# Kernel tuning notes

Measured on AMD Instinct MI355X. Metric: run time of the kernel, lower is better.

Reference implementation:

```python
import jax, jax.numpy as jnp
import numpy as np

B, N, CIN, COUT, K, P = 32, 3072, 32, 8, 3, 4
N2 = N // P


def _lap(key, n):
    a = jax.random.normal(key, (n, n), dtype=jnp.float32)
    # symmetric, spectral radius ~1 (Chebyshev-rescaled Laplacian stand-in)
    return 0.35 * (a + a.T) / jnp.sqrt(jnp.float32(n))


def setup_inputs() -> dict:
    key = jax.random.key(0)
    ks = iter(jax.random.split(key, 40))
    d = {}
    d['x'] = jax.random.normal(next(ks), (B, N, CIN), dtype=jnp.float32)
    d['L0'] = _lap(next(ks), N)
    d['L1'] = _lap(next(ks), N2)

    def cheb_p(k, cin, cout):
        w = jax.random.normal(k, (K, cin, cout), dtype=jnp.float32) * (1.0 / np.sqrt(K * cin))
        return w, jnp.zeros((cout,), jnp.float32)

    def bn_p(c):
        return jnp.ones((c,), jnp.float32), jnp.zeros((c,), jnp.float32)

    d['w11'], d['b11'] = cheb_p(next(ks), CIN, 64); d['g11'], d['be11'] = bn_p(64)
    d['w13'], d['b13'] = cheb_p(next(ks), 64, 128); d['g13'], d['be13'] = bn_p(128)
    d['wr1'] = jax.random.normal(next(ks), (128, CIN), dtype=jnp.float32) * (1.0 / np.sqrt(CIN))
    d['br1'] = jnp.zeros((128,), jnp.float32)
    d['w21'], d['b21'] = cheb_p(next(ks), 128, 192); d['g21'], d['be21'] = bn_p(192)
    d['w23'], d['b23'] = cheb_p(next(ks), 192, 128); d['g23'], d['be23'] = bn_p(128)
    d['wr2'] = jax.random.normal(next(ks), (128, 128), dtype=jnp.float32) * (1.0 / np.sqrt(128))
    d['br2'] = jnp.zeros((128,), jnp.float32)
    d['uw11'], d['ub11'] = cheb_p(next(ks), 256, 128); d['ug11'], d['ube11'] = bn_p(128)
    d['uw12'], d['ub12'] = cheb_p(next(ks), 128, 64); d['ug12'], d['ube12'] = bn_p(64)
    d['uwr1'] = jax.random.normal(next(ks), (64, 256), dtype=jnp.float32) * (1.0 / np.sqrt(256))
    d['ubr1'] = jnp.zeros((64,), jnp.float32)
    d['uw13'], d['ub13'] = cheb_p(next(ks), 64, COUT)
    return d


def cheb_conv(x, L, W, b):
    # x: [B,n,Cin], L: [n,n], W: [K,Cin,Cout] -> [B,n,Cout]
    x0 = x
    x1 = jnp.einsum('ij,bjc->bic', L, x0)
    xs = [x0, x1]
    for _ in range(2, K):
        xs.append(2.0 * jnp.einsum('ij,bjc->bic', L, xs[-1]) - xs[-2])
    xk = jnp.stack(xs, axis=2)  # [B,n,K,Cin]
    return jnp.einsum('bnkc,kco->bno', xk, W) + b


def bn_relu(y, g, be, eps=1e-5):
    mu = jnp.mean(y, axis=(0, 1), keepdims=True)
    var = jnp.mean(jnp.square(y - mu), axis=(0, 1), keepdims=True)
    return jax.nn.relu((y - mu) * jax.lax.rsqrt(var + eps) * g + be)


def lin1x1(x, W, b):
    # torch Conv1d(cin,cout,1) on [B,C,N] == per-node linear
    return jnp.einsum('bnc,oc->bno', x, W) + b


def pool_max(x):
    b, n, c = x.shape
    r = x.reshape(b, n // P, P, c)
    loc = jnp.argmax(r, axis=2)                       # [B,n/P,C]
    vals = jnp.max(r, axis=2)
    idx = loc + (jnp.arange(n // P) * P)[None, :, None]
    return vals, idx


def unpool_max(vals, idx, n):
    b, np_, c = vals.shape
    out = jnp.zeros((b, n, c), vals.dtype)
    bi = jnp.arange(b)[:, None, None]
    ci = jnp.arange(c)[None, None, :]
    return out.at[bi, idx, ci].set(vals)


def reference(x, L0, L1, w11, b11, g11, be11, w13, b13, g13, be13, wr1, br1,
              w21, b21, g21, be21, w23, b23, g23, be23, wr2, br2,
              uw11, ub11, ug11, ube11, uw12, ub12, ug12, ube12, uwr1, ubr1,
              uw13, ub13):
    e1 = bn_relu(cheb_conv(x, L0, w11, b11), g11, be11)
    e1 = bn_relu(cheb_conv(e1, L0, w13, b13), g13, be13)
    e1 = e1 + lin1x1(x, wr1, br1)
    p, idx1 = pool_max(e1)
    e2 = bn_relu(cheb_conv(p, L1, w21, b21), g21, be21)
    e2 = bn_relu(cheb_conv(e2, L1, w23, b23), g23, be23)
    e2 = e2 + lin1x1(p, wr2, br2)
    u = unpool_max(e2, idx1, N)
    cat = jnp.concatenate([u, e1], axis=2)            # [B,N,256]
    d = bn_relu(cheb_conv(cat, L0, uw11, ub11), ug11, ube11)
    d = bn_relu(cheb_conv(d, L0, uw12, ub12), ug12, ube12)
    d = d + lin1x1(cat, uwr1, ubr1)
    return cheb_conv(d, L0, uw13, ub13)               # [B,N,COUT]
```

## Files before the change

kernel.cpp:

```cpp
#include <hip/hip_runtime.h>

typedef _Float16 f16;
typedef f16    half8 __attribute__((ext_vector_type(8)));
typedef float  f32x4 __attribute__((ext_vector_type(4)));
typedef double f64x4 __attribute__((ext_vector_type(4)));

#define LDH 40

template <int MODE>
__global__ __launch_bounds__(256) void gemm_h(
    const f16* __restrict__ A, const f16* __restrict__ Bg, void* __restrict__ Cg,
    int M, int K, int N, int ldc, long long sB, long long sC, int KS)
{
    const int gz   = blockIdx.z / KS;
    const int sl   = blockIdx.z - gz * KS;
    const int Ks   = K / KS;
    const int kbeg = sl * Ks;

    const f16* B = Bg + (size_t)gz * sB;

    __shared__ f16 Ah[128][LDH];
    __shared__ f16 Bt[128][LDH];

    const int tid  = threadIdx.x;
    const int lane = tid & 63;
    const int wv   = tid >> 6;
    const int wm   = wv >> 1, wn = wv & 1;
    const int ln   = lane & 15;
    const int q    = lane >> 4;

    const int row0 = blockIdx.y * 128;
    const int col0 = blockIdx.x * 128;

    const int am = tid >> 1;
    const int ak = (tid & 1) << 4;
    const int bk = tid >> 3;
    const int bn = (tid & 7) << 4;

    const f16* Arow = A + (size_t)(row0 + am) * K + kbeg + ak;
    const int  cb   = col0 + bn;

    f32x4 acc[4][4];
#pragma unroll
    for (int i = 0; i < 4; ++i)
#pragma unroll
        for (int j = 0; j < 4; ++j) acc[i][j] = (f32x4){0.f, 0.f, 0.f, 0.f};

    uint4 a0 = *(const uint4*)(Arow);
    uint4 a1 = *(const uint4*)(Arow + 8);
    uint4 b0 = make_uint4(0, 0, 0, 0), b1 = make_uint4(0, 0, 0, 0);
    {
        const f16* Brow = B + (size_t)(kbeg + bk) * N;
        if (cb + 8  <= N) b0 = *(const uint4*)(Brow + cb);
        if (cb + 16 <= N) b1 = *(const uint4*)(Brow + cb + 8);
    }

    for (int k0 = 0; k0 < Ks; k0 += 32) {
        __syncthreads();
        *(uint4*)&Ah[am][ak]     = a0;
        *(uint4*)&Ah[am][ak + 8] = a1;
        {
            const f16* h0 = (const f16*)&b0;
            const f16* h1 = (const f16*)&b1;
#pragma unroll
            for (int j = 0; j < 8; ++j) {
                int n = bn + j;
                Bt[n][bk ^ (((n >> 4) & 3) << 3)] = h0[j];
            }
#pragma unroll
            for (int j = 0; j < 8; ++j) {
                int n = bn + 8 + j;
                Bt[n][bk ^ (((n >> 4) & 3) << 3)] = h1[j];
            }
        }
        __syncthreads();

        if (k0 + 32 < Ks) {
            a0 = *(const uint4*)(Arow + k0 + 32);
            a1 = *(const uint4*)(Arow + k0 + 40);
            const f16* Brow = B + (size_t)(kbeg + k0 + 32 + bk) * N;
            if (cb + 8  <= N) b0 = *(const uint4*)(Brow + cb);
            if (cb + 16 <= N) b1 = *(const uint4*)(Brow + cb + 8);
        }

        half8 af[4], bf[4];
#pragma unroll
        for (int i = 0; i < 4; ++i)
            af[i] = *(const half8*)&Ah[wm * 64 + i * 16 + ln][q * 8];
#pragma unroll
        for (int j = 0; j < 4; ++j) {
            const int nb = wn * 64 + j * 16 + ln;
            const int sw = ((wn * 4 + j) & 3) << 3;
            bf[j] = *(const half8*)&Bt[nb][(q * 8) ^ sw];
        }
#pragma unroll
        for (int i = 0; i < 4; ++i)
#pragma unroll
            for (int j = 0; j < 4; ++j)
                acc[i][j] = __builtin_amdgcn_mfma_f32_16x16x32_f16(af[i], bf[j], acc[i][j], 0, 0, 0);
    }

    const size_t zoff = (size_t)gz * sC;
#pragma unroll
    for (int i = 0; i < 4; ++i) {
#pragma unroll
        for (int j = 0; j < 4; ++j) {
            const int c = col0 + wn * 64 + j * 16 + ln;
            if (c < N) {
#pragma unroll
                for (int t = 0; t < 4; ++t) {
                    const int r = row0 + wm * 64 + i * 16 + q * 4 + t;
                    const size_t o = zoff + (size_t)r * ldc + c;
                    const float v = acc[i][j][t];
                    if (MODE == 0)      ((f16*)Cg)[o] = (f16)v;
                    else if (MODE == 1) ((float*)Cg)[o] = v;
                    else if (MODE == 2) ((float*)Cg)[o] += v;
                    else                atomicAdd(&((float*)Cg)[o], v);
                }
            }
        }
    }
}

__global__ void probe_f64_k(int* __restrict__ tbl) {
    int l = threadIdx.x & 63;
    f64x4 z = (f64x4){0.0, 0.0, 0.0, 0.0};
    f64x4 dA = __builtin_amdgcn_mfma_f64_16x16x4f64((double)l, 1.0, z, 0, 0, 0);
    f64x4 dB = __builtin_amdgcn_mfma_f64_16x16x4f64(1.0, (double)l, z, 0, 0, 0);
    int* t = tbl + l * 12;
    {
        int v = (int)dA[0];
        if ((v & 3) == 0) { t[0] = l & 15; t[1] = l >> 4; }
        else              { t[0] = l >> 2; t[1] = l & 3;  }
    }
    {
        int v = (int)dB[0];
        if ((v & 3) == 0) { t[2] = l & 15; t[3] = l >> 4; }
        else              { t[2] = l >> 2; t[3] = l & 3;  }
    }
#pragma unroll
    for (int r = 0; r < 4; ++r) {
        int vA = (int)dA[r];
        t[4 + r] = ((vA & 3) == 0) ? (vA - 96) / 4 : (vA - 6) / 16;
        int vB = (int)dB[r];
        t[8 + r] = ((vB & 3) == 0) ? (vB - 96) / 4 : (vB - 6) / 16;
    }
}

__device__ inline void loadA4(const float* p, double* d) {
    float4 v = *(const float4*)p;
    d[0] = v.x; d[1] = v.y; d[2] = v.z; d[3] = v.w;
}
__device__ inline void loadA4(const double* p, double* d) {
    double2 v0 = *(const double2*)p, v1 = *(const double2*)(p + 2);
    d[0] = v0.x; d[1] = v0.y; d[2] = v1.x; d[3] = v1.y;
}

#define LDD 66

template <typename TA>
__global__ __launch_bounds__(256) void gemm_f64(
    const TA* __restrict__ A, const double* __restrict__ Bg, double* __restrict__ Cg,
    const int* __restrict__ tbl,
    int M, int K, int N, long long sB, long long sC, int accum)
{
    const double* B = Bg + (size_t)blockIdx.z * sB;
    double*       C = Cg + (size_t)blockIdx.z * sC;

    __shared__ double As[16][LDD];
    __shared__ double Bs[16][LDD];

    const int tid  = threadIdx.x;
    const int lane = tid & 63;
    const int wv   = tid >> 6;
    const int m0   = wv << 4;

    const int* tl = tbl + lane * 12;
    const int mA = tl[0], kA = tl[1], nB = tl[2], kB = tl[3];
    int iT[4], jT[4];
#pragma unroll
    for (int r = 0; r < 4; ++r) { iT[r] = tl[4 + r]; jT[r] = tl[8 + r]; }

    const int row0 = blockIdx.y * 64;
    const int col0 = blockIdx.x * 64;

    const int ra = tid >> 2;
    const int ka = (tid & 3) << 2;
    const int kb = tid >> 4;
    const int cb = (tid & 15) << 2;

    const TA* Arow = A + (size_t)(row0 + ra) * K + ka;
    const int cbase = col0 + cb;

    f64x4 acc[4];
#pragma unroll
    for (int j = 0; j < 4; ++j) acc[j] = (f64x4){0.0, 0.0, 0.0, 0.0};

    double av[4];
    double2 bv0 = {0.0, 0.0}, bv1 = {0.0, 0.0};
    loadA4(Arow, av);
    if (cbase < N) {
        bv0 = *(const double2*)(B + (size_t)kb * N + cbase);
        bv1 = *(const double2*)(B + (size_t)kb * N + cbase + 2);
    }

    for (int k0 = 0; k0 < K; k0 += 16) {
        __syncthreads();
        As[ka + 0][ra] = av[0]; As[ka + 1][ra] = av[1];
        As[ka + 2][ra] = av[2]; As[ka + 3][ra] = av[3];
        *(double2*)&Bs[kb][cb]     = bv0;
        *(double2*)&Bs[kb][cb + 2] = bv1;
        __syncthreads();

        if (k0 + 16 < K) {
            loadA4(Arow + k0 + 16, av);
            if (cbase < N) {
                bv0 = *(const double2*)(B + (size_t)(k0 + 16 + kb) * N + cbase);
                bv1 = *(const double2*)(B + (size_t)(k0 + 16 + kb) * N + cbase + 2);
            }
        }

#pragma unroll
        for (int kq = 0; kq < 4; ++kq) {
            const double a = As[(kq << 2) + kA][m0 + mA];
#pragma unroll
            for (int j = 0; j < 4; ++j) {
                const double b = Bs[(kq << 2) + kB][(j << 4) + nB];
                acc[j] = __builtin_amdgcn_mfma_f64_16x16x4f64(a, b, acc[j], 0, 0, 0);
            }
        }
    }

#pragma unroll
    for (int j = 0; j < 4; ++j) {
#pragma unroll
        for (int r = 0; r < 4; ++r) {
            const int c = col0 + (j << 4) + jT[r];
            if (c < N) {
                const int rr = row0 + m0 + iT[r];
                double* p = C + (size_t)rr * N + c;
                double v = acc[j][r];
                if (accum) v += *p;
                *p = v;
            }
        }
    }
}

__global__ __launch_bounds__(256) void gemm_f64n(
    const float* __restrict__ A, const double* __restrict__ Bg, double* __restrict__ Cg,
    const int* __restrict__ tbl,
    int M, int K, int N, long long sB, long long sC)
{
    const double* B = Bg + (size_t)blockIdx.z * sB;
    double*       C = Cg + (size_t)blockIdx.z * sC;

    __shared__ double As[16][66];
    __shared__ double Bs[16][34];

    const int tid  = threadIdx.x;
    const int lane = tid & 63;
    const int wv   = tid >> 6;
    const int m0   = wv << 4;

    const int* tl = tbl + lane * 12;
    const int mA = tl[0], kA = tl[1], nB = tl[2], kB = tl[3];
    int iT[4], jT[4];
#pragma unroll
    for (int r = 0; r < 4; ++r) { iT[r] = tl[4 + r]; jT[r] = tl[8 + r]; }

    const int row0 = blockIdx.y * 64;
    const int col0 = blockIdx.x * 32;

    const int ra = tid >> 2;
    const int ka = (tid & 3) << 2;
    const int kb = tid >> 4;
    const int cb = (tid & 15) << 1;

    const float* Arow = A + (size_t)(row0 + ra) * K + ka;
    const int cbase = col0 + cb;

    f64x4 acc[2];
#pragma unroll
    for (int j = 0; j < 2; ++j) acc[j] = (f64x4){0.0, 0.0, 0.0, 0.0};

    double av[4];
    double2 bv = {0.0, 0.0};
    loadA4(Arow, av);
    if (cbase < N) bv = *(const double2*)(B + (size_t)kb * N + cbase);

    for (int k0 = 0; k0 < K; k0 += 16) {
        __syncthreads();
        As[ka + 0][ra] = av[0]; As[ka + 1][ra] = av[1];
        As[ka + 2][ra] = av[2]; As[ka + 3][ra] = av[3];
        *(double2*)&Bs[kb][cb] = bv;
        __syncthreads();

        if (k0 + 16 < K) {
            loadA4(Arow + k0 + 16, av);
            if (cbase < N) bv = *(const double2*)(B + (size_t)(k0 + 16 + kb) * N + cbase);
        }

#pragma unroll
        for (int kq = 0; kq < 4; ++kq) {
            const double a = As[(kq << 2) + kA][m0 + mA];
#pragma unroll
            for (int j = 0; j < 2; ++j) {
                const double b = Bs[(kq << 2) + kB][(j << 4) + nB];
                acc[j] = __builtin_amdgcn_mfma_f64_16x16x4f64(a, b, acc[j], 0, 0, 0);
            }
        }
    }

#pragma unroll
    for (int j = 0; j < 2; ++j) {
#pragma unroll
        for (int r = 0; r < 4; ++r) {
            const int c = col0 + (j << 4) + jT[r];
            if (c < N) {
                const int rr = row0 + m0 + iT[r];
                C[(size_t)rr * N + c] = acc[j][r];
            }
        }
    }
}

__global__ void zero_k(float* __restrict__ p, int n) {
    int i = blockIdx.x * blockDim.x + threadIdx.x;
    if (i < n) p[i] = 0.f;
}

__global__ void cast16_k(const float* __restrict__ s, f16* __restrict__ d, int n) {
    int i = blockIdx.x * blockDim.x + threadIdx.x;
    if (i < n) d[i] = (f16)s[i];
}

__global__ void regroup_in64_k(const float* __restrict__ x, double* __restrict__ XT, int total) {
    int i = blockIdx.x * blockDim.x + threadIdx.x;
    if (i >= total) return;
    int c = i & 31;
    int t = i >> 5;
    int n = t % 3072;
    int b = t / 3072;
    XT[((((size_t)(b >> 3) * 3072 + n) << 3) + (b & 7)) * 32 + c] = (double)x[i];
}

__global__ void cheb_combine16_k(const float* __restrict__ w, f16* __restrict__ wa,
                                 f16* __restrict__ wb, f16* __restrict__ wc, int n) {
    int i = blockIdx.x * blockDim.x + threadIdx.x;
    if (i >= n) return;
    float w0 = w[i], w1 = w[n + i], w2 = w[2 * n + i];
    wa[i] = (f16)(w0 - w2); wb[i] = (f16)w1; wc[i] = (f16)(2.f * w2);
}
__global__ void cheb_combine64_k(const float* __restrict__ w, double* __restrict__ wa,
                                 double* __restrict__ wb, double* __restrict__ wc, int n) {
    int i = blockIdx.x * blockDim.x + threadIdx.x;
    if (i >= n) return;
    double w0 = w[i], w1 = w[n + i], w2 = w[2 * n + i];
    wa[i] = w0 - w2; wb[i] = w1; wc[i] = 2.0 * w2;
}

__global__ void transpose_w16_k(const float* __restrict__ w, f16* __restrict__ wt, int R, int Ccol) {
    int i = blockIdx.x * blockDim.x + threadIdx.x;
    if (i >= R * Ccol) return;
    int r = i / Ccol, c = i - r * Ccol;
    wt[(size_t)c * R + r] = (f16)w[i];
}
__global__ void transpose_w64_k(const float* __restrict__ w, double* __restrict__ wt, int R, int Ccol) {
    int i = blockIdx.x * blockDim.x + threadIdx.x;
    if (i >= R * Ccol) return;
    int r = i / Ccol, c = i - r * Ccol;
    wt[(size_t)c * R + r] = (double)w[i];
}

__global__ void bn_reduce_k(const float* __restrict__ X, float* __restrict__ stats,
                            int rows, int ld, int off) {
    int c = threadIdx.x;
    float s = 0.f, s2 = 0.f;
    for (int r = blockIdx.x; r < rows; r += gridDim.x) {
        float v = X[(size_t)r * ld + off + c];
        s += v; s2 += v * v;
    }
    atomicAdd(&stats[c], s);
    atomicAdd(&stats[256 + c], s2);
}
__global__ void bn_apply_k(float* X, const float* __restrict__ stats,
                           const float* __restrict__ g, const float* __restrict__ be,
                           const float* rbias, f16* mirror,
                           int total, int C, float invN, int ld, int off) {
    int i = blockIdx.x * blockDim.x + threadIdx.x;
    if (i >= total) return;
    int c = i % C;
    int row = i / C;
    size_t a = (size_t)row * ld + off + c;
    float mu = stats[c] * invN;
    float var = stats[256 + c] * invN - mu * mu;
    float sc = g[c] * rsqrtf(var + 1e-5f);
    float v = (X[a] - mu) * sc + be[c];
    v = fmaxf(v, 0.f);
    if (rbias) v += rbias[c];
    X[a] = v;
    if (mirror) mirror[a] = (f16)v;
}

__global__ void bn_reduce64_k(const double* __restrict__ X, double* __restrict__ stats,
                              int rows, int ld) {
    int c = threadIdx.x;
    double s = 0.0, s2 = 0.0;
    for (int r = blockIdx.x; r < rows; r += gridDim.x) {
        double v = X[(size_t)r * ld + c];
        s += v; s2 += v * v;
    }
    atomicAdd(&stats[c], s);
    atomicAdd(&stats[256 + c], s2);
}
__global__ void bn_apply64_k(double* X, const double* __restrict__ stats,
                             const float* __restrict__ g, const float* __restrict__ be,
                             const float* rbias, int total, int C, double invN) {
    int i = blockIdx.x * blockDim.x + threadIdx.x;
    if (i >= total) return;
    int c = i % C;
    double mu = stats[c] * invN;
    double var = stats[256 + c] * invN - mu * mu;
    double sc = (double)g[c] / sqrt(var + 1e-5);
    double v = (X[i] - mu) * sc + (double)be[c];
    v = v > 0.0 ? v : 0.0;
    if (rbias) v += (double)rbias[c];
    X[i] = v;
}

__global__ void cast_e1_k(const double* __restrict__ E1, f16* __restrict__ cat, int total) {
    int i = blockIdx.x * blockDim.x + threadIdx.x;
    if (i >= total) return;
    int c = i & 127;
    int row = i >> 7;
    cat[(size_t)row * 256 + 128 + c] = (f16)E1[i];
}

__global__ void pool4_64_k(const double* __restrict__ e1, f16* __restrict__ p,
                           int* __restrict__ idx, int total) {
    int i = blockIdx.x * blockDim.x + threadIdx.x;
    if (i >= total) return;
    int c = i & 127;
    int t = i >> 7;
    int b = t & 7;
    t >>= 3;
    int q = t % 768;
    int g = t / 768;
    size_t base = ((((size_t)g * 3072 + 4 * q) << 3) + b) * 128 + c;
    double best = e1[base];
    int bj = 0;
#pragma unroll
    for (int j = 1; j < 4; ++j) {
        double v = e1[base + (size_t)j * 1024];
        if (v > best) { best = v; bj = j; }
    }
    p[i] = (f16)best;
    idx[i] = 4 * q + bj;
}

__global__ void unpool_cat_k(const float* __restrict__ e2, const int* __restrict__ idx,
                             f16* __restrict__ cat, int total) {
    int i = blockIdx.x * blockDim.x + threadIdx.x;
    if (i >= total) return;
    int c = i & 127;
    int t = i >> 7;
    int b = t & 7;
    t >>= 3;
    int q = t % 768;
    int g = t / 768;
    f16 val = (f16)e2[i];
    int id = idx[i];
    size_t base = ((((size_t)g * 3072 + 4 * q) << 3) + b) * 256 + c;
#pragma unroll
    for (int j = 0; j < 4; ++j)
        cat[base + (size_t)j * 2048] = (4 * q + j == id) ? val : (f16)0.f;
}

__global__ void transpose_out_k(const float* __restrict__ O, const float* __restrict__ bias,
                                float* __restrict__ out, int total) {
    int i = blockIdx.x * blockDim.x + threadIdx.x;
    if (i >= total) return;
    int c = i & 7;
    int t = i >> 3;
    int n = t % 3072;
    int b = t / 3072;
    out[i] = O[((((size_t)(b >> 3) * 3072 + n) << 3) + (b & 7)) * 8 + c] + bias[c];
}

extern "C" void kernel_launch(void* const* d_in, const int* in_sizes, int n_in,
                              void* d_out, int out_size, void* d_ws, size_t ws_size,
                              hipStream_t stream)
{
    (void)in_sizes; (void)n_in; (void)out_size; (void)ws_size;

    const float* x    = (const float*)d_in[0];
    const float* L0   = (const float*)d_in[1];
    const float* L1   = (const float*)d_in[2];
    const float* w11  = (const float*)d_in[3];
    const float* g11  = (const float*)d_in[5];
    const float* be11 = (const float*)d_in[6];
    const float* w13  = (const float*)d_in[7];
    const float* g13  = (const float*)d_in[9];
    const float* be13 = (const float*)d_in[10];
    const float* wr1  = (const float*)d_in[11];
    const float* br1  = (const float*)d_in[12];
    const float* w21  = (const float*)d_in[13];
    const float* g21  = (const float*)d_in[15];
    const float* be21 = (const float*)d_in[16];
    const float* w23  = (const float*)d_in[17];
    const float* g23  = (const float*)d_in[19];
    const float* be23 = (const float*)d_in[20];
    const float* wr2  = (const float*)d_in[21];
    const float* br2  = (const float*)d_in[22];
    const float* uw11 = (const float*)d_in[23];
    const float* ug11 = (const float*)d_in[25];
    const float* ube11= (const float*)d_in[26];
    const float* uw12 = (const float*)d_in[27];
    const float* ug12 = (const float*)d_in[29];
    const float* ube12= (const float*)d_in[30];
    const float* uwr1 = (const float*)d_in[31];
    const float* ubr1 = (const float*)d_in[32];
    const float* uw13 = (const float*)d_in[33];
    const float* ub13 = (const float*)d_in[34];
    float* out = (float*)d_out;

    float* ws = (float*)d_ws;
    size_t off = 0;
    auto alloc = [&](size_t n) { float* p = ws + off; off += (n + 63) & ~(size_t)63; return p; };

    float* R1 = alloc(12582912);
    float* R2 = alloc(25165824);
    float* R3 = alloc(6291456);
    float* R4 = alloc(6291456);
    int*  IDX = (int*)alloc(3145728);
    float* L0f = alloc(4718592);
    float* L1f = alloc(294912);
    float* ST  = alloc(1536);
    int*  TBL  = (int*)alloc(768);

    f16* wa21h = (f16*)alloc(12288); f16* wb21h = (f16*)alloc(12288); f16* wc21h = (f16*)alloc(12288);
    f16* wa23h = (f16*)alloc(12288); f16* wb23h = (f16*)alloc(12288); f16* wc23h = (f16*)alloc(12288);
    f16* wau11h = (f16*)alloc(16384); f16* wbu11h = (f16*)alloc(16384); f16* wcu11h = (f16*)alloc(16384);
    f16* wau12h = (f16*)alloc(4096);  f16* wbu12h = (f16*)alloc(4096);  f16* wcu12h = (f16*)alloc(4096);
    f16* wau13h = (f16*)alloc(256);   f16* wbu13h = (f16*)alloc(256);   f16* wcu13h = (f16*)alloc(256);
    f16* wr2Th  = (f16*)alloc(8192);
    f16* uwr1Th = (f16*)alloc(8192);

    double* wa11_64 = (double*)alloc(4096);
    double* wb11_64 = (double*)alloc(4096);
    double* wc11_64 = (double*)alloc(4096);
    double* wa13_64 = (double*)alloc(16384);
    double* wb13_64 = (double*)alloc(16384);
    double* wc13_64 = (double*)alloc(16384);
    double* wr1T_64 = (double*)alloc(8192);

    f16*    CATh = (f16*)R1;
    double* H1   = (double*)R1;
    float*  D1   = R2;
    float*  H2   = R2;
    float*  Y3   = R2 + 4718592;
    float*  O    = R2;
    float*  H64  = R2 + 12582912;
    f16*    T1h  = (f16*)(R2 + 18874368);
    f16*    T2h  = (f16*)(R2 + 22020096);
    f16*    TCMB = T1h;
    double* E1   = (double*)R2;
    double* XT64 = (double*)R3;
    f16*    H2h  = (f16*)R3;
    f16*    D1h  = (f16*)R3;
    double* T1d  = (double*)R4;
    double* T2d  = (double*)IDX;
    f16*    Ph   = (f16*)R4;
    f16*    H64h = (f16*)(R4 + 1572864);
    f16*    L0h  = (f16*)L0f;
    f16*    L1h  = (f16*)L1f;
    double* ST64 = (double*)(ST + 512);
    float*  RFa  = H64;
    float*  RFb  = R2;

    auto gh = [&](int mode, const f16* A, const f16* B, void* C, int M, int K, int N,
                  int ldc, long long sB, long long sC, int z, int ks) {
        dim3 grid((N + 127) / 128, M / 128, z * ks);
        if (mode == 0)      gemm_h<0><<<grid, 256, 0, stream>>>(A, B, C, M, K, N, ldc, sB, sC, ks);
        else if (mode == 1) gemm_h<1><<<grid, 256, 0, stream>>>(A, B, C, M, K, N, ldc, sB, sC, ks);
        else if (mode == 2) gemm_h<2><<<grid, 256, 0, stream>>>(A, B, C, M, K, N, ldc, sB, sC, ks);
        else                gemm_h<3><<<grid, 256, 0, stream>>>(A, B, C, M, K, N, ldc, sB, sC, ks);
    };
    auto gemm64f = [&](const float* A, const double* B, double* C, int M, int K, int N,
                       long long sB, long long sC, int z) {
        dim3 grid((N + 31) / 32, M / 64, z);
        gemm_f64n<<<grid, 256, 0, stream>>>(A, B, C, TBL, M, K, N, sB, sC);
    };
    auto gemm64d = [&](const double* A, const double* B, double* C, int M, int K, int N, int accum) {
        dim3 grid((N + 63) / 64, M / 64);
        gemm_f64<double><<<grid, 256, 0, stream>>>(A, B, C, TBL, M, K, N, 0, 0, accum);
    };
    auto bn = [&](float* X, int rows, int C, int ld, int offc,
                  const float* gp, const float* bep, const float* rbias, f16* mirror) {
        zero_k<<<2, 256, 0, stream>>>(ST, 512);
        bn_reduce_k<<<384, C, 0, stream>>>(X, ST, rows, ld, offc);
        int total = rows * C;
        bn_apply_k<<<(total + 255) / 256, 256, 0, stream>>>(
            X, ST, gp, bep, rbias, mirror, total, C, 1.f / (float)rows, ld, offc);
    };
    auto bn64 = [&](double* X, int rows, int C,
                    const float* gp, const float* bep, const float* rbias) {
        zero_k<<<4, 256, 0, stream>>>(ST + 512, 1024);
        bn_reduce64_k<<<384, C, 0, stream>>>(X, ST64, rows, C);
        int total = rows * C;
        bn_apply64_k<<<(total + 255) / 256, 256, 0, stream>>>(
            X, ST64, gp, bep, rbias, total, C, 1.0 / (double)rows);
    };
    auto comb16 = [&](const float* w, f16* a, f16* b, f16* c, int n) {
        cheb_combine16_k<<<(n + 255) / 256, 256, 0, stream>>>(w, a, b, c, n);
    };

    probe_f64_k<<<1, 64, 0, stream>>>(TBL);

    cheb_combine64_k<<<8, 256, 0, stream>>>(w11, wa11_64, wb11_64, wc11_64, 2048);
    cheb_combine64_k<<<32, 256, 0, stream>>>(w13, wa13_64, wb13_64, wc13_64, 8192);
    transpose_w64_k<<<16, 256, 0, stream>>>(wr1, wr1T_64, 128, 32);
    regroup_in64_k<<<12288, 256, 0, stream>>>(x, XT64, 3145728);

    gemm64f(L0, XT64, T1d, 3072, 3072, 256, 786432, 786432, 4);
    gemm64f(L0, T1d, T2d, 3072, 3072, 256, 786432, 786432, 4);
    gemm64d(XT64, wa11_64, H1, 98304, 32, 64, 0);
    gemm64d(T1d,  wb11_64, H1, 98304, 32, 64, 1);
    gemm64d(T2d,  wc11_64, H1, 98304, 32, 64, 1);
    bn64(H1, 98304, 64, g11, be11, nullptr);

    for (int h = 0; h < 2; ++h) {
        const double* Hh = H1 + (size_t)h * 3145728;
        double*       Eh = E1 + (size_t)h * 6291456;
        gemm64f(L0, Hh, T1d, 3072, 3072, 512, 1572864, 1572864, 2);
        gemm64f(L0, T1d, T2d, 3072, 3072, 512, 1572864, 1572864, 2);
        gemm64d(Hh,  wa13_64, Eh, 49152, 64, 128, 0);
        gemm64d(T1d, wb13_64, Eh, 49152, 64, 128, 1);
        gemm64d(T2d, wc13_64, Eh, 49152, 64, 128, 1);
    }
    bn64(E1, 98304, 128, g13, be13, br1);
    gemm64d(XT64, wr1T_64, E1, 98304, 32, 128, 1);

    comb16(w21,  wa21h,  wb21h,  wc21h,  24576);
    comb16(w23,  wa23h,  wb23h,  wc23h,  24576);
    comb16(uw11, wau11h, wbu11h, wcu11h, 32768);
    comb16(uw12, wau12h, wbu12h, wcu12h, 8192);
    comb16(uw13, wau13h, wbu13h, wcu13h, 512);
    transpose_w16_k<<<64, 256, 0, stream>>>(wr2, wr2Th, 128, 128);
    transpose_w16_k<<<64, 256, 0, stream>>>(uwr1, uwr1Th, 64, 256);
    cast16_k<<<36864, 256, 0, stream>>>(L0, L0h, 9437184);
    cast16_k<<<2304, 256, 0, stream>>>(L1, L1h, 589824);

    pool4_64_k<<<12288, 256, 0, stream>>>(E1, Ph, IDX, 3145728);
    cast_e1_k<<<49152, 256, 0, stream>>>(E1, CATh, 12582912);

    gh(0, L1h, Ph, T1h, 768, 768, 1024, 1024, 786432, 786432, 4, 1);
    gh(0, L1h, T1h, T2h, 768, 768, 1024, 1024, 786432, 786432, 4, 1);
    gh(1, Ph,  wa21h, H2, 24576, 128, 192, 192, 0, 0, 1, 1);
    gh(2, T1h, wb21h, H2, 24576, 128, 192, 192, 0, 0, 1, 1);
    gh(2, T2h, wc21h, H2, 24576, 128, 192, 192, 0, 0, 1, 1);
    bn(H2, 24576, 192, 192, 0, g21, be21, nullptr, H2h);

    gh(0, L1h, H2h, T1h, 768, 768, 1536, 1536, 1179648, 1179648, 4, 1);
    gh(0, L1h, T1h, T2h, 768, 768, 1536, 1536, 1179648, 1179648, 4, 1);
    gh(1, H2h, wa23h, Y3, 24576, 192, 128, 128, 0, 0, 1, 1);
    gh(2, T1h, wb23h, Y3, 24576, 192, 128, 128, 0, 0, 1, 1);
    gh(2, T2h, wc23h, Y3, 24576, 192, 128, 128, 0, 0, 1, 1);
    bn(Y3, 24576, 128, 128, 0, g23, be23, br2, nullptr);
    gh(2, Ph, wr2Th, Y3, 24576, 128, 128, 128, 0, 0, 1, 1);

    unpool_cat_k<<<12288, 256, 0, stream>>>(Y3, IDX, CATh, 3145728);

    gh(0, CATh, wcu11h, TCMB, 98304, 256, 128, 128, 0, 0, 1, 1);
    gh(1, CATh, wbu11h, RFb, 98304, 256, 128, 128, 0, 0, 1, 1);
    gh(2, L0h, TCMB, RFb, 3072, 3072, 1024, 1024, 3145728, 3145728, 4, 1);
    cast16_k<<<49152, 256, 0, stream>>>(RFb, TCMB, 12582912);
    gh(1, CATh, wau11h, D1, 98304, 256, 128, 128, 0, 0, 1, 1);
    gh(2, L0h, TCMB, D1, 3072, 3072, 1024, 1024, 3145728, 3145728, 4, 1);
    bn(D1, 98304, 128, 128, 0, ug11, ube11, nullptr, D1h);

    gh(0, D1h, wcu12h, T2h, 98304, 128, 64, 64, 0, 0, 1, 1);
    gh(1, D1h, wbu12h, RFb, 98304, 128, 64, 64, 0, 0, 1, 1);
    gh(3, L0h, T2h, RFb, 3072, 3072, 512, 512, 1572864, 1572864, 4, 2);
    cast16_k<<<24576, 256, 0, stream>>>(RFb, T1h, 6291456);
    gh(1, D1h, wau12h, H64, 98304, 128, 64, 64, 0, 0, 1, 1);
    gh(3, L0h, T1h, H64, 3072, 3072, 512, 512, 1572864, 1572864, 4, 2);
    bn(H64, 98304, 64, 64, 0, ug12, ube12, ubr1, nullptr);
    gh(2, CATh, uwr1Th, H64, 98304, 256, 64, 64, 0, 0, 1, 1);
    cast16_k<<<24576, 256, 0, stream>>>(H64, H64h, 6291456);

    gh(0, H64h, wcu13h, T2h, 98304, 64, 8, 8, 0, 0, 1, 1);
    gh(1, H64h, wbu13h, RFa, 98304, 64, 8, 8, 0, 0, 1, 1);
    gh(3, L0h, T2h, RFa, 3072, 3072, 64, 64, 196608, 196608, 4, 8);
    cast16_k<<<3072, 256, 0, stream>>>(RFa, T1h, 786432);
    gh(1, H64h, wau13h, O, 98304, 64, 8, 8, 0, 0, 1, 1);
    gh(3, L0h, T1h, O, 3072, 3072, 64, 64, 196608, 196608, 4, 8);

    transpose_out_k<<<3072, 256, 0, stream>>>(O, ub13, out, 786432);
}
```

Measured before the change: 4.055 ms.

## Fuse three Chebyshev weight GEMMs into one f64 kernel; split-K the L1 propagations

Adds a double-precision MFMA GEMM that walks a concatenated K dimension over the three Chebyshev terms (x, T1, T2) and their weights. It writes C once, which replaces three launches that each read and re-wrote the output. The L1 Laplacian propagations now use split-K (4 slices) with an atomic or accumulate mode into a float scratch buffer, followed by a cast to fp16. This raises occupancy on the small 768x768 GEMMs, at the cost of extra zero and cast passes and more global traffic.

```diff
diff --git a/kernel.cpp b/kernel.cpp
--- a/kernel.cpp
+++ b/kernel.cpp
@@ -242,6 +242,101 @@
                 double v = acc[j][r];
                 if (accum) v += *p;
                 *p = v;
+            }
+        }
+    }
+}
+
+__global__ __launch_bounds__(256) void gemm_f64w3(
+    const double* __restrict__ A0g, const double* __restrict__ A1g, const double* __restrict__ A2g,
+    const double* __restrict__ B0g, const double* __restrict__ B1g, const double* __restrict__ B2g,
+    double* __restrict__ C, const int* __restrict__ tbl,
+    int M, int K, int N)
+{
+    (void)M;
+    __shared__ double As[16][LDD];
+    __shared__ double Bs[16][LDD];
+
+    const int tid  = threadIdx.x;
+    const int lane = tid & 63;
+    const int wv   = tid >> 6;
+    const int m0   = wv << 4;
+
+    const int* tl = tbl + lane * 12;
+    const int mA = tl[0], kA = tl[1], nB = tl[2], kB = tl[3];
+    int iT[4], jT[4];
+#pragma unroll
+    for (int r = 0; r < 4; ++r) { iT[r] = tl[4 + r]; jT[r] = tl[8 + r]; }
+
+    const int row0 = blockIdx.y * 64;
+    const int col0 = blockIdx.x * 64;
+
+    const int ra = tid >> 2;
+    const int ka = (tid & 3) << 2;
+    const int kb = tid >> 4;
+    const int cb = (tid & 15) << 2;
+
+    const size_t aoff = (size_t)(row0 + ra) * K + ka;
+    const double* Ar0 = A0g + aoff;
+    const double* Ar1 = A1g + aoff;
+    const double* Ar2 = A2g + aoff;
+    const int cbase = col0 + cb;
+
+    f64x4 acc[4];
+#pragma unroll
+    for (int j = 0; j < 4; ++j) acc[j] = (f64x4){0.0, 0.0, 0.0, 0.0};
+
+    const int KT = 3 * K;
+    double av[4];
+    double2 bv0 = {0.0, 0.0}, bv1 = {0.0, 0.0};
+    loadA4(Ar0, av);
+    if (cbase < N) {
+        const double* Brow = B0g + (size_t)kb * N + cbase;
+        bv0 = *(const double2*)Brow;
+        bv1 = *(const double2*)(Brow + 2);
+    }
+
+    for (int kt = 0; kt < KT; kt += 16) {
+        __syncthreads();
+        As[ka + 0][ra] = av[0]; As[ka + 1][ra] = av[1];
+        As[ka + 2][ra] = av[2]; As[ka + 3][ra] = av[3];
+        *(double2*)&Bs[kb][cb]     = bv0;
+        *(double2*)&Bs[kb][cb + 2] = bv1;
+        __syncthreads();
+
+        const int nt = kt + 16;
+        if (nt < KT) {
+            const int m    = (nt >= 2 * K) ? 2 : ((nt >= K) ? 1 : 0);
+            const int koff = nt - m * K;
+            const double* Ap = (m == 0) ? Ar0 : ((m == 1) ? Ar1 : Ar2);
+            const double* Bp = (m == 0) ? B0g : ((m == 1) ? B1g : B2g);
+            loadA4(Ap + koff, av);
+            if (cbase < N) {
+                const double* Brow = Bp + (size_t)(koff + kb) * N + cbase;
+                bv0 = *(const double2*)Brow;
+                bv1 = *(const double2*)(Brow + 2);
+            }
+        }
+
+#pragma unroll
+        for (int kq = 0; kq < 4; ++kq) {
+            const double a = As[(kq << 2) + kA][m0 + mA];
+#pragma unroll
+            for (int j = 0; j < 4; ++j) {
+                const double b = Bs[(kq << 2) + kB][(j << 4) + nB];
+                acc[j] = __builtin_amdgcn_mfma_f64_16x16x4f64(a, b, acc[j], 0, 0, 0);
+            }
+        }
+    }
+
+#pragma unroll
+    for (int j = 0; j < 4; ++j) {
+#pragma unroll
+        for (int r = 0; r < 4; ++r) {
+            const int c = col0 + (j << 4) + jT[r];
+            if (c < N) {
+                const int rr = row0 + m0 + iT[r];
+                C[(size_t)rr * N + c] = acc[j][r];
             }
         }
     }
@@ -578,6 +673,7 @@
     double* ST64 = (double*)(ST + 512);
     float*  RFa  = H64;
     float*  RFb  = R2;
+    float*  FSCR = H64;
 
     auto gh = [&](int mode, const f16* A, const f16* B, void* C, int M, int K, int N,
                   int ldc, long long sB, long long sC, int z, int ks) {
@@ -595,6 +691,12 @@
     auto gemm64d = [&](const double* A, const double* B, double* C, int M, int K, int N, int accum) {
         dim3 grid((N + 63) / 64, M / 64);
         gemm_f64<double><<<grid, 256, 0, stream>>>(A, B, C, TBL, M, K, N, 0, 0, accum);
+    };
+    auto gemm64w3 = [&](const double* A0, const double* A1, const double* A2,
+                        const double* B0, const double* B1, const double* B2,
+                        double* C, int M, int K, int N) {
+        dim3 grid((N + 63) / 64, M / 64);
+        gemm_f64w3<<<grid, 256, 0, stream>>>(A0, A1, A2, B0, B1, B2, C, TBL, M, K, N);
     };
     auto bn = [&](float* X, int rows, int C, int ld, int offc,
                   const float* gp, const float* bep, const float* rbias, f16* mirror) {
@@ -625,9 +727,7 @@
 
     gemm64f(L0, XT64, T1d, 3072, 3072, 256, 786432, 786432, 4);
     gemm64f(L0, T1d, T2d, 3072, 3072, 256, 786432, 786432, 4);
-    gemm64d(XT64, wa11_64, H1, 98304, 32, 64, 0);
-    gemm64d(T1d,  wb11_64, H1, 98304, 32, 64, 1);
-    gemm64d(T2d,  wc11_64, H1, 98304, 32, 64, 1);
+    gemm64w3(XT64, T1d, T2d, wa11_64, wb11_64, wc11_64, H1, 98304, 32, 64);
     bn64(H1, 98304, 64, g11, be11, nullptr);
 
     for (int h = 0; h < 2; ++h) {
@@ -635,9 +735,7 @@
         double*       Eh = E1 + (size_t)h * 6291456;
         gemm64f(L0, Hh, T1d, 3072, 3072, 512, 1572864, 1572864, 2);
         gemm64f(L0, T1d, T2d, 3072, 3072, 512, 1572864, 1572864, 2);
-        gemm64d(Hh,  wa13_64, Eh, 49152, 64, 128, 0);
-        gemm64d(T1d, wb13_64, Eh, 49152, 64, 128, 1);
-        gemm64d(T2d, wc13_64, Eh, 49152, 64, 128, 1);
+        gemm64w3(Hh, T1d, T2d, wa13_64, wb13_64, wc13_64, Eh, 49152, 64, 128);
     }
     bn64(E1, 98304, 128, g13, be13, br1);
     gemm64d(XT64, wr1T_64, E1, 98304, 32, 128, 1);
@@ -655,15 +753,23 @@
     pool4_64_k<<<12288, 256, 0, stream>>>(E1, Ph, IDX, 3145728);
     cast_e1_k<<<49152, 256, 0, stream>>>(E1, CATh, 12582912);
 
-    gh(0, L1h, Ph, T1h, 768, 768, 1024, 1024, 786432, 786432, 4, 1);
-    gh(0, L1h, T1h, T2h, 768, 768, 1024, 1024, 786432, 786432, 4, 1);
+    zero_k<<<12288, 256, 0, stream>>>(FSCR, 3145728);
+    gh(3, L1h, Ph, FSCR, 768, 768, 1024, 1024, 786432, 786432, 4, 4);
+    cast16_k<<<12288, 256, 0, stream>>>(FSCR, T1h, 3145728);
+    zero_k<<<12288, 256, 0, stream>>>(FSCR, 3145728);
+    gh(3, L1h, T1h, FSCR, 768, 768, 1024, 1024, 786432, 786432, 4, 4);
+    cast16_k<<<12288, 256, 0, stream>>>(FSCR, T2h, 3145728);
     gh(1, Ph,  wa21h, H2, 24576, 128, 192, 192, 0, 0, 1, 1);
     gh(2, T1h, wb21h, H2, 24576, 128, 192, 192, 0, 0, 1, 1);
     gh(2, T2h, wc21h, H2, 24576, 128, 192, 192, 0, 0, 1, 1);
     bn(H2, 24576, 192, 192, 0, g21, be21, nullptr, H2h);
 
-    gh(0, L1h, H2h, T1h, 768, 768, 1536, 1536, 1179648, 1179648, 4, 1);
-    gh(0, L1h, T1h, T2h, 768, 768, 1536, 1536, 1179648, 1179648, 4, 1);
+    zero_k<<<18432, 256, 0, stream>>>(FSCR, 4718592);
+    gh(3, L1h, H2h, FSCR, 768, 768, 1536, 1536, 1179648, 1179648, 4, 4);
+    cast16_k<<<18432, 256, 0, stream>>>(FSCR, T1h, 4718592);
+    zero_k<<<18432, 256, 0, stream>>>(FSCR, 4718592);
+    gh(3, L1h, T1h, FSCR, 768, 768, 1536, 1536, 1179648, 1179648, 4, 4);
+    cast16_k<<<18432, 256, 0, stream>>>(FSCR, T2h, 4718592);
     gh(1, H2h, wa23h, Y3, 24576, 192, 128, 128, 0, 0, 1, 1);
     gh(2, T1h, wb23h, Y3, 24576, 192, 128, 128, 0, 0, 1, 1);
     gh(2, T2h, wc23h, Y3, 24576, 192, 128, 128, 0, 0, 1, 1);
```

New measurement: 4.126 ms. No clear change (+1.8%).
